# Optimization experiments

Hardware: AMD Instinct MI355X
Metric: run time of the kernel (lower is better)

Reference implementation:

```python
import jax, jax.numpy as jnp
import numpy as np

B, S = 128, 512          # batch, padded expression length
D = 256                  # kos/identifier embedding dim (asserted equal)
KIND_D = 8               # token-kind embedding dim
EXPR_D = 512             # expression_encoding_dim
KOS_VOCAB = 256
KIND_VOCAB = 8
NUM_IDS = 8192
PAD_IDX = 0              # padding_idx -> zero embedding row
IDENTIFIER_KIND = 3
KOS_KINDS = (4, 5, 6)    # OPERATOR, SEPARATOR, KEYWORD


def setup_inputs() -> dict:
    key = jax.random.key(0)
    ks = jax.random.split(key, 8)
    token_type = jax.random.randint(ks[0], (B, S), 0, KIND_VOCAB, dtype=jnp.int32)
    kos_token_index = jax.random.randint(ks[1], (B * S,), 0, KOS_VOCAB, dtype=jnp.int32)
    identifier_indices = jax.random.randint(ks[2], (B * S,), 0, NUM_IDS, dtype=jnp.int32)
    encoded_identifiers = jax.random.normal(ks[3], (NUM_IDS, D), jnp.float32)
    kind_emb = jax.random.normal(ks[4], (KIND_VOCAB, KIND_D), jnp.float32).at[PAD_IDX].set(0.0)
    kos_emb = jax.random.normal(ks[5], (KOS_VOCAB, D), jnp.float32).at[PAD_IDX].set(0.0)
    sp = 1.0 / np.sqrt(KIND_D + D)
    W_proj = jax.random.uniform(ks[6], (KIND_D + D, EXPR_D), jnp.float32, -sp, sp)
    b_proj = jnp.zeros((EXPR_D,), jnp.float32)
    sa = 1.0 / np.sqrt(EXPR_D)
    W_add = jax.random.uniform(ks[7], (EXPR_D, EXPR_D), jnp.float32, -sa, sa)
    b_add = jnp.zeros((EXPR_D,), jnp.float32)
    return {
        'token_type': token_type,
        'kos_token_index': kos_token_index,
        'identifier_indices': identifier_indices,
        'encoded_identifiers': encoded_identifiers,
        'kind_emb': kind_emb,
        'kos_emb': kos_emb,
        'W_proj': W_proj,
        'b_proj': b_proj,
        'W_add': W_add,
        'b_add': b_add,
    }


def reference(token_type, kos_token_index, identifier_indices, encoded_identifiers,
              kind_emb, kos_emb, W_proj, b_proj, W_add, b_add):
    # token-kind embedding lookup: [B, S, KIND_D]
    kind_e = kind_emb[token_type]

    flat_kind = token_type.reshape(-1)                       # [B*S]
    is_id = flat_kind == IDENTIFIER_KIND
    is_kos = (flat_kind == KOS_KINDS[0]) | (flat_kind == KOS_KINDS[1]) | (flat_kind == KOS_KINDS[2])

    # embedding-table gathers (sources for masked_scatter, consumed in order)
    id_src = encoded_identifiers[identifier_indices]         # [B*S, D]
    kos_src = kos_emb[kos_token_index]                       # [B*S, D]

    # masked_scatter semantics: the k-th True position gets the k-th source row
    rank_id = jnp.maximum(jnp.cumsum(is_id) - 1, 0)
    rank_kos = jnp.maximum(jnp.cumsum(is_kos) - 1, 0)
    enc = jnp.where(is_id[:, None], id_src[rank_id], jnp.float32(0.0))
    enc = jnp.where(is_kos[:, None], kos_src[rank_kos], enc)
    enc = enc.reshape(B, S, D)

    # concat + 2-layer MLP (dropout is identity in eval mode)
    x = jnp.concatenate([kind_e, enc], axis=-1)              # [B, S, KIND_D + D]
    x = jax.nn.relu(x @ W_proj + b_proj)                     # [B, S, EXPR_D]
    x = jax.nn.relu(x @ W_add + b_add)                       # [B, S, EXPR_D]
    return x
```

## Files before the change

kernel.cpp:

```cpp
#include <hip/hip_runtime.h>
#include <hip/hip_bf16.h>

#define BB 128
#define SS 512
#define NPOS (BB*SS)
#define DD 256
#define KIND_D 8
#define EXPR_D 512
#define KOS_VOCAB 256
#define NUM_IDS 8192
#define IDENTIFIER_KIND 3
#define TROWS 9088

typedef unsigned short u16;
typedef __attribute__((ext_vector_type(8))) short s16x8;
typedef __attribute__((ext_vector_type(8))) unsigned short u16x8;
typedef __attribute__((ext_vector_type(4))) float f32x4;

__device__ __forceinline__ u16 bf16bits(float v) {
    __hip_bfloat16 h = __float2bfloat16(v);
    return *(u16*)&h;
}
__device__ __forceinline__ float bf16tof(u16 b) {
    __hip_bfloat16 h = *(__hip_bfloat16*)&b;
    return __bfloat162float(h);
}

__global__ __launch_bounds__(256) void prep_kernel(const float* __restrict__ W2,
                                                   const float* __restrict__ kind_emb,
                                                   const float* __restrict__ Wp,
                                                   const float* __restrict__ bp,
                                                   const int* __restrict__ token_type,
                                                   u16* __restrict__ Wt,
                                                   u16* __restrict__ Wt1,
                                                   float* __restrict__ kindc,
                                                   int2* __restrict__ blkcnt) {
    __shared__ float tile[32][33];
    __shared__ int swid[4], swkos[4];
    const int bi = blockIdx.x;
    const int t = threadIdx.x;

    if (bi < 256) {
        const int n0 = (bi & 15) * 32;
        const int k0 = (bi >> 4) * 32;
        const int lj = t & 31, li = t >> 5;
        #pragma unroll
        for (int p = 0; p < 4; ++p) {
            int i = li + p * 8;
            tile[i][lj] = W2[(size_t)(k0 + i) * EXPR_D + n0 + lj];
        }
        __syncthreads();
        #pragma unroll
        for (int p = 0; p < 4; ++p) {
            int j = li + p * 8;
            Wt[(size_t)(n0 + j) * EXPR_D + k0 + lj] = bf16bits(tile[lj][j]);
        }
    } else if (bi == 256) {
        #pragma unroll
        for (int rep = 0; rep < 2; ++rep) {
            int j = t + rep * 256;
            float bias = bp[j];
            for (int kind = 0; kind < 8; ++kind) {
                float a = bias;
                #pragma unroll
                for (int d = 0; d < KIND_D; ++d)
                    a = fmaf(kind_emb[kind * KIND_D + d], Wp[d * EXPR_D + j], a);
                kindc[kind * EXPR_D + j] = a;
            }
        }
    } else if (bi < 385) {
        const int idx = bi - 257;
        const int n0 = (idx & 15) * 32;
        const int k0 = (idx >> 4) * 32;
        const float* W1p = Wp + (size_t)KIND_D * EXPR_D;
        const int lj = t & 31, li = t >> 5;
        #pragma unroll
        for (int p = 0; p < 4; ++p) {
            int i = li + p * 8;
            tile[i][lj] = W1p[(size_t)(k0 + i) * EXPR_D + n0 + lj];
        }
        __syncthreads();
        #pragma unroll
        for (int p = 0; p < 4; ++p) {
            int j = li + p * 8;
            Wt1[(size_t)(n0 + j) * DD + k0 + lj] = bf16bits(tile[lj][j]);
        }
    } else {
        const int blk = bi - 385;
        const int lane = t & 63, wave = t >> 6;
        int k = token_type[blk * 256 + t];
        unsigned long long mid  = __ballot(k == IDENTIFIER_KIND);
        unsigned long long mkos = __ballot(k >= 4 && k <= 6);
        if (lane == 0) { swid[wave] = __popcll(mid); swkos[wave] = __popcll(mkos); }
        __syncthreads();
        if (t == 0) {
            int a = 0, c = 0;
            #pragma unroll
            for (int w = 0; w < 4; ++w) { a += swid[w]; c += swkos[w]; }
            blkcnt[blk] = make_int2(a, c);
        }
    }
}

__global__ __launch_bounds__(256) void scatter_kernel(const int* __restrict__ token_type,
                                                      const int2* __restrict__ blkcnt,
                                                      const int* __restrict__ kos_idx,
                                                      const int* __restrict__ id_idx,
                                                      int* __restrict__ sel2) {
    __shared__ int2 sbase;
    __shared__ int swid[4], swkos[4];
    const int b = blockIdx.x, t = threadIdx.x;
    const int lane = t & 63, wave = t >> 6;
    if (t < 64) {
        int a = 0, c = 0;
        for (int i = t; i < b; i += 64) { int2 v = blkcnt[i]; a += v.x; c += v.y; }
        #pragma unroll
        for (int off = 32; off; off >>= 1) { a += __shfl_down(a, off); c += __shfl_down(c, off); }
        if (t == 0) sbase = make_int2(a, c);
    }
    const int idx = b * 256 + t;
    const int k = token_type[idx];
    const bool fid  = (k == IDENTIFIER_KIND);
    const bool fkos = (k >= 4 && k <= 6);
    unsigned long long mid  = __ballot(fid);
    unsigned long long mkos = __ballot(fkos);
    if (lane == 0) { swid[wave] = __popcll(mid); swkos[wave] = __popcll(mkos); }
    __syncthreads();
    int bid = 0, bkos = 0;
    for (int w = 0; w < wave; ++w) { bid += swid[w]; bkos += swkos[w]; }
    unsigned long long below = (1ull << lane) - 1ull;
    int s;
    if (fid)       s = id_idx[sbase.x + bid + __popcll(mid & below)];
    else if (fkos) s = 8192 + (k - 4) * 256 + kos_idx[sbase.y + bkos + __popcll(mkos & below)];
    else           s = 8960 + k;
    sel2[idx] = s;
}

__global__ __launch_bounds__(512, 2) void table_kernel(const float* __restrict__ enc_ids,
                                                       const float* __restrict__ kos_emb,
                                                       const u16* __restrict__ Wt1,
                                                       const float* __restrict__ kindc,
                                                       u16* __restrict__ Thi) {
    __shared__ u16 sAhi[2][128 * 64];
    __shared__ u16 sAlo[2][128 * 64];
    __shared__ u16 sB[2][256 * 64];

    const int t = threadIdx.x;
    const int row0 = blockIdx.x * 128;
    const int col0 = blockIdx.y * 256;

    const int ar = t >> 2;
    const int ac = (t & 3) * 16;
    const int br = t >> 1;
    const int bc = (t & 1) * 32;

    const int arow = row0 + ar;
    const float* Arow;
    bool hasrc = true;
    if (arow < NUM_IDS)        Arow = &enc_ids[(size_t)arow * DD];
    else if (arow < 8960)      Arow = &kos_emb[(size_t)((arow - NUM_IDS) & 255) * DD];
    else { Arow = enc_ids; hasrc = false; }
    const u16* Brow = &Wt1[(size_t)(col0 + br) * DD];

    const int lane = t & 63;
    const int wid  = t >> 6;
    const int wr = wid >> 2, wc = wid & 3;
    const int lrow = lane & 15, lkg = lane >> 4;

    f32x4 acc[4][4];
    #pragma unroll
    for (int mi = 0; mi < 4; ++mi)
        #pragma unroll
        for (int ni = 0; ni < 4; ++ni)
            acc[mi][ni] = (f32x4){0.f, 0.f, 0.f, 0.f};

    f32x4 av[4];
    u16x8 bv[4];

    auto STAGE_ISSUE = [&](int kc) {
        const int kb = kc * 64;
        #pragma unroll
        for (int j = 0; j < 4; ++j)
            av[j] = hasrc ? *(const f32x4*)&Arow[kb + ac + j * 4] : (f32x4){0.f,0.f,0.f,0.f};
        #pragma unroll
        for (int j = 0; j < 4; ++j) bv[j] = *(const u16x8*)&Brow[kb + bc + j * 8];
    };

    auto WRITE = [&](int buf) {
        u16 hi[16], lo[16];
        #pragma unroll
        for (int j = 0; j < 4; ++j)
            #pragma unroll
            for (int e = 0; e < 4; ++e) {
                float r = av[j][e];
                u16 h = bf16bits(r);
                hi[j * 4 + e] = h;
                lo[j * 4 + e] = bf16bits(r - bf16tof(h));
            }
        const int abase = ar * 128;
        const int o0 = abase + ((ac * 2) ^ ((ar & 7) << 4));
        const int o1 = abase + ((ac * 2 + 16) ^ ((ar & 7) << 4));
        *(u16x8*)((char*)sAhi[buf] + o0) = *(const u16x8*)&hi[0];
        *(u16x8*)((char*)sAhi[buf] + o1) = *(const u16x8*)&hi[8];
        *(u16x8*)((char*)sAlo[buf] + o0) = *(const u16x8*)&lo[0];
        *(u16x8*)((char*)sAlo[buf] + o1) = *(const u16x8*)&lo[8];
        const int bbase = br * 128;
        #pragma unroll
        for (int j = 0; j < 4; ++j) {
            int off = bbase + ((bc * 2 + j * 16) ^ ((br & 7) << 4));
            *(u16x8*)((char*)sB[buf] + off) = bv[j];
        }
    };

    auto COMPUTE = [&](int buf) {
        #pragma unroll
        for (int ks = 0; ks < 2; ++ks) {
            s16x8 ah[4], al[4], bbf[4];
            #pragma unroll
            for (int mi = 0; mi < 4; ++mi) {
                int row = wr * 64 + mi * 16 + lrow;
                int off = row * 128 + ((ks * 64 + lkg * 16) ^ ((row & 7) << 4));
                ah[mi] = *(const s16x8*)((const char*)sAhi[buf] + off);
                al[mi] = *(const s16x8*)((const char*)sAlo[buf] + off);
            }
            #pragma unroll
            for (int ni = 0; ni < 4; ++ni) {
                int row = wc * 64 + ni * 16 + lrow;
                int off = row * 128 + ((ks * 64 + lkg * 16) ^ ((row & 7) << 4));
                bbf[ni] = *(const s16x8*)((const char*)sB[buf] + off);
            }
            #pragma unroll
            for (int mi = 0; mi < 4; ++mi)
                #pragma unroll
                for (int ni = 0; ni < 4; ++ni) {
                    acc[mi][ni] = __builtin_amdgcn_mfma_f32_16x16x32_bf16(ah[mi], bbf[ni], acc[mi][ni], 0, 0, 0);
                    acc[mi][ni] = __builtin_amdgcn_mfma_f32_16x16x32_bf16(al[mi], bbf[ni], acc[mi][ni], 0, 0, 0);
                }
        }
    };

    STAGE_ISSUE(0);
    WRITE(0);
    __syncthreads();
    int cur = 0;
    #pragma unroll 1
    for (int kc = 0; kc < 4; ++kc) {
        if (kc < 3) STAGE_ISSUE(kc + 1);
        COMPUTE(cur);
        if (kc < 3) WRITE(cur ^ 1);
        __syncthreads();
        cur ^= 1;
    }

    #pragma unroll
    for (int ni = 0; ni < 4; ++ni) {
        int col = col0 + wc * 64 + ni * 16 + lrow;
        #pragma unroll
        for (int mi = 0; mi < 4; ++mi) {
            int rbase = row0 + wr * 64 + mi * 16 + lkg * 4;
            #pragma unroll
            for (int j = 0; j < 4; ++j) {
                int rg = rbase + j;
                int kind = (rg < NUM_IDS) ? 3
                         : (rg < 8960) ? 4 + ((rg - NUM_IDS) >> 8)
                         : (rg < 8968) ? (rg - 8960) : 0;
                float v = acc[mi][ni][j] + kindc[kind * EXPR_D + col];
                Thi[(size_t)rg * EXPR_D + col] = bf16bits(fmaxf(v, 0.f));
            }
        }
    }
}

__global__ __launch_bounds__(512, 4) void mlp2_kernel(const int* __restrict__ sel2,
                                                      const u16* __restrict__ Thi,
                                                      const u16* __restrict__ Wt,
                                                      const float* __restrict__ b2,
                                                      float* __restrict__ out) {
    __shared__ u16 sA[2][128 * 32];
    __shared__ u16 sB[2][256 * 32];

    const int t = threadIdx.x;
    const int row0 = blockIdx.x * 128;
    const int col0 = blockIdx.y * 256;

    const int ar = t >> 2;
    const int ac8 = (t & 3) * 8;
    const int br = t >> 1;
    const int bc16 = (t & 1) * 16;

    const int trow = sel2[row0 + ar];
    const u16* Arow = &Thi[(size_t)trow * EXPR_D + ac8];
    const u16* Brow = &Wt[(size_t)(col0 + br) * EXPR_D + bc16];

    const int lane = t & 63;
    const int wid  = t >> 6;
    const int wr = wid >> 2, wc = wid & 3;
    const int lrow = lane & 15, lkg = lane >> 4;

    f32x4 acc[4][4];
    #pragma unroll
    for (int mi = 0; mi < 4; ++mi)
        #pragma unroll
        for (int ni = 0; ni < 4; ++ni)
            acc[mi][ni] = (f32x4){0.f, 0.f, 0.f, 0.f};

    u16x8 av;
    u16x8 bv[2];

    auto STAGE_ISSUE = [&](int kc) {
        const int kb = kc * 32;
        av = *(const u16x8*)&Arow[kb];
        bv[0] = *(const u16x8*)&Brow[kb];
        bv[1] = *(const u16x8*)&Brow[kb + 8];
    };

    auto WRITE = [&](int buf) {
        int aoff = ar * 64 + ((ac8 * 2) ^ ((ar & 3) << 4));
        *(u16x8*)((char*)sA[buf] + aoff) = av;
        #pragma unroll
        for (int j = 0; j < 2; ++j) {
            int boff = br * 64 + ((bc16 * 2 + j * 16) ^ ((br & 3) << 4));
            *(u16x8*)((char*)sB[buf] + boff) = bv[j];
        }
    };

    auto COMPUTE = [&](int buf) {
        s16x8 a[4], b[4];
        #pragma unroll
        for (int mi = 0; mi < 4; ++mi) {
            int row = wr * 64 + mi * 16 + lrow;
            int off = row * 64 + ((lkg * 16) ^ ((row & 3) << 4));
            a[mi] = *(const s16x8*)((const char*)sA[buf] + off);
        }
        #pragma unroll
        for (int ni = 0; ni < 4; ++ni) {
            int row = wc * 64 + ni * 16 + lrow;
            int off = row * 64 + ((lkg * 16) ^ ((row & 3) << 4));
            b[ni] = *(const s16x8*)((const char*)sB[buf] + off);
        }
        #pragma unroll
        for (int mi = 0; mi < 4; ++mi)
            #pragma unroll
            for (int ni = 0; ni < 4; ++ni)
                acc[mi][ni] = __builtin_amdgcn_mfma_f32_16x16x32_bf16(a[mi], b[ni], acc[mi][ni], 0, 0, 0);
    };

    STAGE_ISSUE(0);
    WRITE(0);
    __syncthreads();
    int cur = 0;
    #pragma unroll 1
    for (int kc = 0; kc < 16; ++kc) {
        if (kc < 15) STAGE_ISSUE(kc + 1);
        COMPUTE(cur);
        if (kc < 15) WRITE(cur ^ 1);
        __syncthreads();
        cur ^= 1;
    }

    #pragma unroll
    for (int ni = 0; ni < 4; ++ni) {
        int col = col0 + wc * 64 + ni * 16 + lrow;
        float bias = b2[col];
        #pragma unroll
        for (int mi = 0; mi < 4; ++mi) {
            int rbase = row0 + wr * 64 + mi * 16 + lkg * 4;
            #pragma unroll
            for (int j = 0; j < 4; ++j)
                out[(size_t)(rbase + j) * EXPR_D + col] = fmaxf(acc[mi][ni][j] + bias, 0.f);
        }
    }
}

extern "C" void kernel_launch(void* const* d_in, const int* in_sizes, int n_in,
                              void* d_out, int out_size, void* d_ws, size_t ws_size,
                              hipStream_t stream) {
    const int*   token_type = (const int*)d_in[0];
    const int*   kos_idx    = (const int*)d_in[1];
    const int*   id_idx     = (const int*)d_in[2];
    const float* enc_ids    = (const float*)d_in[3];
    const float* kind_emb   = (const float*)d_in[4];
    const float* kos_emb    = (const float*)d_in[5];
    const float* Wp         = (const float*)d_in[6];
    const float* bp         = (const float*)d_in[7];
    const float* W2         = (const float*)d_in[8];
    const float* b2         = (const float*)d_in[9];
    float* out = (float*)d_out;

    char* ws = (char*)d_ws;
    int*   sel2   = (int*)ws;
    float* kindc  = (float*)(ws + 262144);
    u16*   Thi    = (u16*)(ws + 278528);
    u16*   Wt     = (u16*)(ws + 9584640);
    u16*   Wt1    = (u16*)(ws + 10108928);
    int2*  blkcnt = (int2*)(ws + 10371072);

    hipLaunchKernelGGL(prep_kernel, dim3(641), dim3(256), 0, stream,
                       W2, kind_emb, Wp, bp, token_type, Wt, Wt1, kindc, blkcnt);
    hipLaunchKernelGGL(scatter_kernel, dim3(256), dim3(256), 0, stream,
                       token_type, blkcnt, kos_idx, id_idx, sel2);
    hipLaunchKernelGGL(table_kernel, dim3(TROWS / 128, EXPR_D / 256), dim3(512), 0, stream,
                       enc_ids, kos_emb, Wt1, kindc, Thi);
    hipLaunchKernelGGL(mlp2_kernel, dim3(NPOS / 128, EXPR_D / 256), dim3(512), 0, stream,
                       sel2, Thi, Wt, b2, out);
}
```

Measured before the change: 82.35 us.

## Precompute second MLP layer over table rows and gather final outputs per position

The second GEMM now runs only over the 9088 unique table rows instead of all 65536 positions, writing an fp32 output table. A new gather kernel copies the selected row for each position into the output using nontemporal vector stores. This removes most of the second-layer matmul FLOPs. In exchange it adds an extra kernel launch and an intermediate table round trip, and the output is now bound by gather bandwidth.

```diff
diff --git a/kernel.cpp b/kernel.cpp
--- a/kernel.cpp
+++ b/kernel.cpp
@@ -271,11 +271,10 @@
     }
 }
 
-__global__ __launch_bounds__(512, 4) void mlp2_kernel(const int* __restrict__ sel2,
-                                                      const u16* __restrict__ Thi,
-                                                      const u16* __restrict__ Wt,
-                                                      const float* __restrict__ b2,
-                                                      float* __restrict__ out) {
+__global__ __launch_bounds__(512, 4) void table2_kernel(const u16* __restrict__ Thi,
+                                                        const u16* __restrict__ Wt,
+                                                        const float* __restrict__ b2,
+                                                        float* __restrict__ O) {
     __shared__ u16 sA[2][128 * 32];
     __shared__ u16 sB[2][256 * 32];
 
@@ -288,8 +287,7 @@
     const int br = t >> 1;
     const int bc16 = (t & 1) * 16;
 
-    const int trow = sel2[row0 + ar];
-    const u16* Arow = &Thi[(size_t)trow * EXPR_D + ac8];
+    const u16* Arow = &Thi[(size_t)(row0 + ar) * EXPR_D + ac8];
     const u16* Brow = &Wt[(size_t)(col0 + br) * EXPR_D + bc16];
 
     const int lane = t & 63;
@@ -367,8 +365,29 @@
             int rbase = row0 + wr * 64 + mi * 16 + lkg * 4;
             #pragma unroll
             for (int j = 0; j < 4; ++j)
-                out[(size_t)(rbase + j) * EXPR_D + col] = fmaxf(acc[mi][ni][j] + bias, 0.f);
-        }
+                O[(size_t)(rbase + j) * EXPR_D + col] = fmaxf(acc[mi][ni][j] + bias, 0.f);
+        }
+    }
+}
+
+__global__ __launch_bounds__(256) void gather_kernel(const int* __restrict__ sel2,
+                                                     const float* __restrict__ O,
+                                                     float* __restrict__ out) {
+    const int t = threadIdx.x;
+    const int lane = t & 63, wave = t >> 6;
+    const int base = blockIdx.x * 16;
+    int rows[4];
+    #pragma unroll
+    for (int i = 0; i < 4; ++i) rows[i] = sel2[base + i * 4 + wave];
+    #pragma unroll
+    for (int i = 0; i < 4; ++i) {
+        const int pos = base + i * 4 + wave;
+        const f32x4* src = (const f32x4*)&O[(size_t)rows[i] * EXPR_D];
+        f32x4* dst = (f32x4*)&out[(size_t)pos * EXPR_D];
+        f32x4 v0 = src[lane];
+        f32x4 v1 = src[lane + 64];
+        __builtin_nontemporal_store(v0, &dst[lane]);
+        __builtin_nontemporal_store(v1, &dst[lane + 64]);
     }
 }
 
@@ -390,10 +409,11 @@
     char* ws = (char*)d_ws;
     int*   sel2   = (int*)ws;
     float* kindc  = (float*)(ws + 262144);
-    u16*   Thi    = (u16*)(ws + 278528);
-    u16*   Wt     = (u16*)(ws + 9584640);
-    u16*   Wt1    = (u16*)(ws + 10108928);
-    int2*  blkcnt = (int2*)(ws + 10371072);
+    int2*  blkcnt = (int2*)(ws + 278528);
+    u16*   Wt     = (u16*)(ws + 282624);
+    u16*   Wt1    = (u16*)(ws + 806912);
+    u16*   Thi    = (u16*)(ws + 1069056);
+    float* O      = (float*)(ws + 10375168);
 
     hipLaunchKernelGGL(prep_kernel, dim3(641), dim3(256), 0, stream,
                        W2, kind_emb, Wp, bp, token_type, Wt, Wt1, kindc, blkcnt);
@@ -401,6 +421,8 @@
                        token_type, blkcnt, kos_idx, id_idx, sel2);
     hipLaunchKernelGGL(table_kernel, dim3(TROWS / 128, EXPR_D / 256), dim3(512), 0, stream,
                        enc_ids, kos_emb, Wt1, kindc, Thi);
-    hipLaunchKernelGGL(mlp2_kernel, dim3(NPOS / 128, EXPR_D / 256), dim3(512), 0, stream,
-                       sel2, Thi, Wt, b2, out);
-}
+    hipLaunchKernelGGL(table2_kernel, dim3(TROWS / 128, EXPR_D / 256), dim3(512), 0, stream,
+                       Thi, Wt, b2, O);
+    hipLaunchKernelGGL(gather_kernel, dim3(NPOS / 16), dim3(256), 0, stream,
+                       sel2, O, out);
+}
```

After: 75.85 us. -7.9%, faster.
